# Performance work log

Hardware: AMD Instinct MI355X
Metric: run time of the kernel (lower is better)

Reference implementation:

```python
import jax, jax.numpy as jnp
import numpy as np
import math

LOG_EPS = -1000.0   # matches LOG_EPS in the torch source
NEG = -1e9          # stand-in for -inf (grad-safe)
T_MIN, T_MAX = 0.1, 1.0
GUMBEL_RATIO = 0.5  # gumbel_temperature_ratio forward arg (scalar float)


def setup_inputs() -> dict:
    key = jax.random.key(0)
    k1, k2, k3 = jax.random.split(key, 3)
    B, I, J, D = 4, 96, 384, 256
    return {
        "text_embeddings": jax.random.normal(k1, (B, I, D), jnp.float32),
        "mel_embeddings": jax.random.normal(k2, (B, J, D), jnp.float32),
        "gumbel_noise_u": jax.random.uniform(k3, (B, I, J), jnp.float32,
                                             minval=1e-6, maxval=1.0 - 1e-6),
        "text_mask": jnp.ones((B, I), dtype=bool),
        "mel_mask": jnp.ones((B, J), dtype=bool),
    }


def _soft_alignment(text_embeddings, mel_embeddings, gumbel_noise_u, text_mask, mel_mask):
    B, I, Dt = text_embeddings.shape
    _, J, Dm = mel_embeddings.shape

    # energy (B, I, J) = bmm / sqrt(D_text * D_mel)
    energy = jnp.einsum('bid,bjd->bij', text_embeddings, mel_embeddings) / math.sqrt(Dt * Dm)
    # gumbel noise + temperature
    temperature = T_MIN + (T_MAX - T_MIN) * GUMBEL_RATIO
    noise = -jnp.log(-jnp.log(gumbel_noise_u))
    energy = (energy + noise) / temperature

    len_t = text_mask.sum(1)  # (B,)
    len_m = mel_mask.sum(1)   # (B,)
    j_idx = jnp.arange(J)

    # invalid triangular mask (B, I, J, K): boundary j must not precede previous boundary k
    tri = j_idx[:, None] < j_idx[None, :]                       # (J, K)
    invalid = (tri[None, None]
               | ~text_mask[:, :, None, None]
               | ~mel_mask[:, None, :, None]
               | ~mel_mask[:, None, None, :])
    # force_assign_last: last text token's boundary forced to the last mel frame
    last_i = jnp.arange(I)[None, :] == (len_t - 1)[:, None]     # (B, I)
    not_last_j = j_idx[None, :] != (len_m - 1)[:, None]         # (B, J)
    invalid = invalid | (last_i[:, :, None, None] & not_last_j[:, None, :, None])

    # log conditional prob P(B_i = j | B_{i-1} = k), normalized over j (axis=2)
    e4 = jnp.where(invalid, LOG_EPS, energy[..., None])         # (B, I, J, K)
    log_cond_prob = e4 - jax.nn.logsumexp(e4, axis=2, keepdims=True)
    # reverse logcumsumexp over j: log P(B_i >= j | B_{i-1} = k)
    geq = jnp.flip(jax.lax.cumlogsumexp(jnp.flip(log_cond_prob, 2), axis=2), 2)
    geq = jnp.where(invalid, LOG_EPS, geq)

    # forward DP: B_ij (B, I+1, J+1), B_ij[:,0,0] = 0
    row0 = jnp.full((B, J + 1), NEG).at[:, 0].set(0.0)
    jj = jnp.arange(1, J + 1)

    def step(prev, inp):
        i, lcp = inp                                            # lcp: (B, J, K=J)
        # B_ij[b,i,j] = lse_k B_ij[b,i-1,k] + log_cond_prob[b,i-1,j-1,k]
        vals = jax.nn.logsumexp(prev[:, None, :-1] + lcp, axis=2)  # (B, J)
        window = (jj >= i) & (jj <= J - I + i + 1)              # only j in [i, J-I+i+1] written
        new = jnp.where(window[None, :], vals, NEG)
        new = jnp.concatenate([jnp.full((B, 1), NEG), new], axis=1)
        return new, new

    _, rows = jax.lax.scan(step, row0,
                           (jnp.arange(1, I + 1), jnp.swapaxes(log_cond_prob, 0, 1)))
    Bij = jnp.concatenate([row0[:, None, :], jnp.swapaxes(rows, 0, 1)], axis=1)  # (B, I+1, J+1)

    prob = Bij[:, :-1, :-1]                                     # (B, I, K)
    # log P(B_{i-1} < j <= B_i) = lse_k prob[b,i,k] + geq[b,i,j,k]
    log_boundary = jax.nn.logsumexp(prob[:, :, None, :] + geq, axis=3)  # (B, I, J)
    return log_boundary


def reference(text_embeddings, mel_embeddings, gumbel_noise_u, text_mask, mel_mask):
    soft = _soft_alignment(text_embeddings, mel_embeddings, gumbel_noise_u,
                           text_mask, mel_mask)
    # expanded text embeddings (B, J, D_text)
    expanded = jnp.einsum('bij,bid->bjd', jnp.exp(soft), text_embeddings)
    return soft, expanded
```

## Files before the change

### kernel.cpp

```cpp
#include <hip/hip_runtime.h>
#include <hip/hip_bf16.h>
#include <math.h>

#define B_ 4
#define I_ 96
#define J_ 384
#define D_ 256
#define NEG_     -1000000000.0f
#define NEGINF_  -3.0e38f
#define INV_TEMP_ (1.0f/0.55f)
#define LOG2E_   1.4426950408889634f
#define LN2_     0.6931471805599453f
#define LOGEPS2_ (-1000.0f*LOG2E_)

__device__ __forceinline__ float lse2(float a, float b) {
    float m = fmaxf(a, b);
    float d = fminf(a, b) - m;
    return m + __log2f(1.0f + __builtin_exp2f(d));
}

template<int CTRL, int RMASK = 0xF>
__device__ __forceinline__ float dpp_id(float x) {
    return __int_as_float(__builtin_amdgcn_update_dpp(
        __float_as_int(NEGINF_), __float_as_int(x), CTRL, RMASK, 0xF, false));
}
__device__ __forceinline__ float rdlane(float x, int l_const) {
    return __int_as_float(__builtin_amdgcn_readlane(__float_as_int(x), l_const));
}

__device__ __forceinline__ float wave_incl_prefix_lse(float x) {
    x = lse2(x, dpp_id<0x111>(x));
    x = lse2(x, dpp_id<0x112>(x));
    x = lse2(x, dpp_id<0x114>(x));
    x = lse2(x, dpp_id<0x118>(x));
    x = lse2(x, dpp_id<0x142, 0xa>(x));
    x = lse2(x, dpp_id<0x143, 0xc>(x));
    return x;
}
__device__ __forceinline__ float wave_incl_suffix_lse(float x, int lane) {
    x = lse2(x, dpp_id<0x101>(x));
    x = lse2(x, dpp_id<0x102>(x));
    x = lse2(x, dpp_id<0x104>(x));
    x = lse2(x, dpp_id<0x108>(x));
    float t1 = rdlane(x, 16), t2 = rdlane(x, 32), t3 = rdlane(x, 48);
    int row = lane >> 4;
    float u23 = lse2(t2, t3);
    float add = (row == 3) ? NEGINF_ : (row == 2) ? t3
              : (row == 1) ? u23 : lse2(t1, u23);
    return lse2(x, add);
}
__device__ __forceinline__ float combine_pre(const float* p, int w) {
    float l01 = lse2(p[0], p[1]);
    float l23 = lse2(p[2], p[3]);
    float P3 = lse2(l01, p[2]);
    float P4 = lse2(l01, l23);
    float P5 = lse2(P4, p[4]);
    return (w == 0) ? NEGINF_ : (w == 1) ? p[0] : (w == 2) ? l01
         : (w == 3) ? P3 : (w == 4) ? P4 : P5;
}
__device__ __forceinline__ float combine_suf(const float* s, int w) {
    float h45 = lse2(s[4], s[5]);
    float h23 = lse2(s[2], s[3]);
    float S3 = lse2(s[3], h45);
    float S2 = lse2(h23, h45);
    float S1 = lse2(s[1], S2);
    return (w == 5) ? NEGINF_ : (w == 4) ? s[5] : (w == 3) ? h45
         : (w == 2) ? S3 : (w == 1) ? S2 : S1;
}

__global__ __launch_bounds__(384) void k_energy(
    const float* __restrict__ text, const float* __restrict__ mel,
    const float* __restrict__ gum, float* __restrict__ Sarr,
    float* __restrict__ Earr)
{
    const int i = blockIdx.x, b = blockIdx.y;
    const int tid = threadIdx.x, lane = tid & 63, w = tid >> 6;
    __shared__ float4 tex4[D_/4];
    __shared__ float wtot[6];

    if (tid < D_/4)
        tex4[tid] = ((const float4*)(text + ((size_t)b*I_ + i)*D_))[tid];
    __syncthreads();

    const int j = tid;
    const float4* mrow = (const float4*)(mel + ((size_t)b*J_ + j)*D_);
    float acc = 0.f;
    #pragma unroll 8
    for (int d4 = 0; d4 < D_/4; ++d4) {
        float4 m4 = mrow[d4];
        float4 t4 = tex4[d4];
        acc += t4.x*m4.x + t4.y*m4.y + t4.z*m4.z + t4.w*m4.w;
    }
    float u = gum[((size_t)b*I_ + i)*J_ + j];
    float noise = -__logf(-__logf(u));
    float e2 = (acc * (1.0f/256.0f) + noise) * (INV_TEMP_ * LOG2E_);

    float sincl = wave_incl_suffix_lse(e2, lane);
    if (lane == 0) wtot[w] = sincl;
    __syncthreads();
    float sw = combine_suf(wtot, w);
    size_t off = ((size_t)b*I_ + i)*J_ + j;
    Sarr[off] = lse2(sincl, sw);
    Earr[off] = e2;
}

__global__ __launch_bounds__(64) void k_dp(
    const float* __restrict__ Sarr, const float* __restrict__ Earr,
    float* __restrict__ prob)
{
    const int b = blockIdx.x;
    const int lane = threadIdx.x;
    const int k0 = lane * 6;
    const float* Sb = Sarr + (size_t)b*I_*J_;
    const float* Eb = Earr + (size_t)b*I_*J_;
    float* Pb = prob + (size_t)b*I_*J_;

    float prev[6];
    #pragma unroll
    for (int t = 0; t < 6; ++t) {
        int k = k0 + t;
        float v0 = (k == 0) ? 0.0f : NEG_;
        prev[t] = v0;
        Pb[k] = v0;
    }

    float SA[6], EA[6], SBf[6], EBf[6];
    #pragma unroll
    for (int t = 0; t < 6; ++t) {
        int k = k0 + t;
        SA[t] = Sb[k];
        EA[t] = Eb[(k == 0) ? 0 : k - 1];
    }
    #pragma unroll
    for (int t = 0; t < 6; ++t) {
        int k = k0 + t;
        SBf[t] = Sb[(size_t)1*J_ + k];
        EBf[t] = Eb[(size_t)1*J_ + ((k == 0) ? 0 : k - 1)];
    }

    auto STEP = [&](int i, float* Sx, float* Ex, int loadrow) {
        float v[6], Ecur[6];
        #pragma unroll
        for (int t = 0; t < 6; ++t) { v[t] = prev[t] - Sx[t]; Ecur[t] = Ex[t]; }
        if (loadrow >= 0) {
            #pragma unroll
            for (int t = 0; t < 6; ++t) {
                int k = k0 + t;
                Sx[t] = Sb[(size_t)loadrow*J_ + k];
                Ex[t] = Eb[(size_t)loadrow*J_ + ((k == 0) ? 0 : k - 1)];
            }
        }
        float p[6];
        p[0] = v[0];
        #pragma unroll
        for (int t = 1; t < 6; ++t) p[t] = lse2(p[t-1], v[t]);
        float inc = wave_incl_prefix_lse(p[5]);
        float pexcl = dpp_id<0x138>(inc);
        float nv[6];
        nv[0] = pexcl + Ecur[0];
        #pragma unroll
        for (int t = 1; t < 6; ++t) nv[t] = lse2(pexcl, p[t-1]) + Ecur[t];
        float* Prow = Pb + (size_t)i*J_;
        #pragma unroll
        for (int t = 0; t < 6; ++t) {
            int k = k0 + t;
            bool win = (k >= i) && (k <= 289 + i);
            float val = win ? nv[t] : NEG_;
            prev[t] = val;
            Prow[k] = val;
        }
    };

    int i = 1;
    for (; i + 1 <= I_-1; i += 2) {
        STEP(i,     SA,  EA,  (i + 1 <= I_-2) ? i + 1 : -1);
        STEP(i + 1, SBf, EBf, (i + 2 <= I_-2) ? i + 2 : -1);
    }
    if (i == I_-1) STEP(i, SA, EA, -1);
}

__global__ __launch_bounds__(384) void k_soft(
    float* __restrict__ probsoft,
    const float* __restrict__ Sarr)
{
    const int i = blockIdx.x, b = blockIdx.y;
    const int tid = threadIdx.x, lane = tid & 63, w = tid >> 6;
    const int j = tid;
    __shared__ float tot[12];
    float* Row = probsoft + ((size_t)b*I_ + i)*J_;
    float p = Row[j];

    if (i == I_-1) {
        float sincl = wave_incl_suffix_lse(p, lane);
        if (lane == 0) tot[w] = sincl;
        __syncthreads();
        float m = tot[0];
        #pragma unroll
        for (int t = 1; t < 6; ++t) m = lse2(m, tot[t]);
        Row[j] = (j == J_-1) ? LN2_ * m : LN2_ * m - 1000.0f;
        return;
    }

    float S6 = Sarr[((size_t)b*I_ + i)*J_ + j];
    float v = p - S6;
    float qincl = wave_incl_prefix_lse(v);
    float tsuf  = wave_incl_suffix_lse(p, lane);
    if (lane == 63) tot[w] = qincl;
    if (lane == 0)  tot[6 + w] = tsuf;
    __syncthreads();
    float pt[6], st[6];
    #pragma unroll
    for (int t = 0; t < 6; ++t) { pt[t] = tot[t]; st[t] = tot[6+t]; }
    float Qful = lse2(combine_pre(pt, w), qincl);
    float Texw = dpp_id<0x130>(tsuf);
    float Texc = lse2(combine_suf(st, w), Texw);
    Row[j] = LN2_ * lse2(Qful + S6, Texc + LOGEPS2_);
}

__global__ __launch_bounds__(256) void k_expand(
    const float* __restrict__ soft, const float* __restrict__ text,
    float* __restrict__ out2)
{
    const int j = blockIdx.x, b = blockIdx.y;
    const int tid = threadIdx.x;
    __shared__ float wsh[I_];
    if (tid < I_) wsh[tid] = __expf(soft[((size_t)b*I_ + tid)*J_ + j]);
    __syncthreads();
    float acc = 0.f;
    const float* tcol = text + (size_t)b*I_*D_ + tid;
    #pragma unroll 8
    for (int i = 0; i < I_; ++i) acc += wsh[i] * tcol[(size_t)i*D_];
    out2[((size_t)b*J_ + j)*D_ + tid] = acc;
}

extern "C" void kernel_launch(void* const* d_in, const int* in_sizes, int n_in,
                              void* d_out, int out_size, void* d_ws, size_t ws_size,
                              hipStream_t stream) {
    const float* text = (const float*)d_in[0];
    const float* mel  = (const float*)d_in[1];
    const float* gum  = (const float*)d_in[2];

    float* out    = (float*)d_out;
    float* soft   = out;
    float* out2   = out + (size_t)B_*I_*J_;
    float* Sarr   = out2;
    float* Earr   = out2 + (size_t)B_*I_*J_;
    float* prob   = soft;

    k_energy<<<dim3(I_, B_), 384, 0, stream>>>(text, mel, gum, Sarr, Earr);
    k_dp    <<<dim3(B_),      64, 0, stream>>>(Sarr, Earr, prob);
    k_soft  <<<dim3(I_, B_), 384, 0, stream>>>(prob, Sarr);
    k_expand<<<dim3(J_, B_), 256, 0, stream>>>(soft, text, out2);
}
```

Baseline: 160.6 us.

## Tile energy and expand kernels, stage DP inputs in LDS as packed fp16

The energy kernel now computes six text rows per block, reusing each mel load across them, and rebuilds the per-row suffix log-sum-exp as an in-lane tree plus a wave scan. The DP kernel first preloads the whole per-batch S/E table into shared memory as packed fp16 pairs, so the serial 95-step recurrence reads from LDS instead of global memory. Its in-lane prefix scan is also reorganised into a shallower tree. The expand kernel handles eight output columns per block, reusing each text load across them. The fp16 storage of S and E lowers precision in the recurrence, and the roughly 147 KB LDS buffer limits the DP kernel to one block per CU.

```diff
diff --git a/kernel.cpp b/kernel.cpp
--- a/kernel.cpp
+++ b/kernel.cpp
@@ -1,5 +1,5 @@
 #include <hip/hip_runtime.h>
-#include <hip/hip_bf16.h>
+#include <hip/hip_fp16.h>
 #include <math.h>
 
 #define B_ 4
@@ -73,48 +73,88 @@
     const float* __restrict__ gum, float* __restrict__ Sarr,
     float* __restrict__ Earr)
 {
-    const int i = blockIdx.x, b = blockIdx.y;
+    const int ib = blockIdx.x * 6, b = blockIdx.y;
     const int tid = threadIdx.x, lane = tid & 63, w = tid >> 6;
-    __shared__ float4 tex4[D_/4];
-    __shared__ float wtot[6];
-
-    if (tid < D_/4)
-        tex4[tid] = ((const float4*)(text + ((size_t)b*I_ + i)*D_))[tid];
+    __shared__ float4 tex4[6][D_/4];
+    __shared__ float e2l[6][J_];
+
+    {
+        int r = tid >> 6, c = tid & 63;
+        tex4[r][c] = ((const float4*)(text + ((size_t)b*I_ + ib + r)*D_))[c];
+    }
     __syncthreads();
 
     const int j = tid;
     const float4* mrow = (const float4*)(mel + ((size_t)b*J_ + j)*D_);
-    float acc = 0.f;
-    #pragma unroll 8
+    float acc[6] = {0.f,0.f,0.f,0.f,0.f,0.f};
+    #pragma unroll 4
     for (int d4 = 0; d4 < D_/4; ++d4) {
         float4 m4 = mrow[d4];
-        float4 t4 = tex4[d4];
-        acc += t4.x*m4.x + t4.y*m4.y + t4.z*m4.z + t4.w*m4.w;
-    }
-    float u = gum[((size_t)b*I_ + i)*J_ + j];
-    float noise = -__logf(-__logf(u));
-    float e2 = (acc * (1.0f/256.0f) + noise) * (INV_TEMP_ * LOG2E_);
-
-    float sincl = wave_incl_suffix_lse(e2, lane);
-    if (lane == 0) wtot[w] = sincl;
-    __syncthreads();
-    float sw = combine_suf(wtot, w);
-    size_t off = ((size_t)b*I_ + i)*J_ + j;
-    Sarr[off] = lse2(sincl, sw);
-    Earr[off] = e2;
-}
-
-__global__ __launch_bounds__(64) void k_dp(
+        #pragma unroll
+        for (int r = 0; r < 6; ++r) {
+            float4 t4 = tex4[r][d4];
+            acc[r] += t4.x*m4.x + t4.y*m4.y + t4.z*m4.z + t4.w*m4.w;
+        }
+    }
+    #pragma unroll
+    for (int r = 0; r < 6; ++r) {
+        float u = gum[((size_t)b*I_ + ib + r)*J_ + j];
+        float noise = -__logf(-__logf(u));
+        e2l[r][j] = (acc[r] * (1.0f/256.0f) + noise) * (INV_TEMP_ * LOG2E_);
+    }
+    __syncthreads();
+
+    const int k0 = lane * 6;
+    float x[6];
+    #pragma unroll
+    for (int t = 0; t < 6; ++t) x[t] = e2l[w][k0 + t];
+    float s1[6], s2[6], sfx[6];
+    #pragma unroll
+    for (int t = 0; t < 5; ++t) s1[t] = lse2(x[t], x[t+1]);
+    s1[5] = x[5];
+    #pragma unroll
+    for (int t = 0; t < 4; ++t) s2[t] = lse2(s1[t], s1[t+2]);
+    s2[4] = s1[4]; s2[5] = s1[5];
+    sfx[0] = lse2(s2[0], s2[4]);
+    sfx[1] = lse2(s2[1], s2[5]);
+    #pragma unroll
+    for (int t = 2; t < 6; ++t) sfx[t] = s2[t];
+    float incl = wave_incl_suffix_lse(sfx[0], lane);
+    float excl = dpp_id<0x130>(incl);
+    size_t rowoff = ((size_t)b*I_ + ib + w)*J_ + k0;
+    #pragma unroll
+    for (int t = 0; t < 6; ++t) {
+        Sarr[rowoff + t] = lse2(sfx[t], excl);
+        Earr[rowoff + t] = x[t];
+    }
+}
+
+__global__ __launch_bounds__(384) void k_dp(
     const float* __restrict__ Sarr, const float* __restrict__ Earr,
     float* __restrict__ prob)
 {
+    __shared__ unsigned int SE[I_*J_];
     const int b = blockIdx.x;
-    const int lane = threadIdx.x;
-    const int k0 = lane * 6;
+    const int tid = threadIdx.x;
     const float* Sb = Sarr + (size_t)b*I_*J_;
     const float* Eb = Earr + (size_t)b*I_*J_;
     float* Pb = prob + (size_t)b*I_*J_;
 
+    {
+        const int k = tid, km1 = (k == 0) ? 0 : k - 1;
+        #pragma unroll 4
+        for (int r = 0; r < I_; ++r) {
+            float s = Sb[(size_t)r*J_ + k];
+            float e = Eb[(size_t)r*J_ + km1];
+            unsigned int u = ((unsigned int)__half_as_ushort(__float2half(e)) << 16)
+                           |  (unsigned int)__half_as_ushort(__float2half(s));
+            SE[r*J_ + k] = u;
+        }
+    }
+    __syncthreads();
+    if (tid >= 64) return;
+
+    const int lane = tid, k0 = lane * 6;
     float prev[6];
     #pragma unroll
     for (int t = 0; t < 6; ++t) {
@@ -123,43 +163,38 @@
         prev[t] = v0;
         Pb[k] = v0;
     }
-
-    float SA[6], EA[6], SBf[6], EBf[6];
-    #pragma unroll
-    for (int t = 0; t < 6; ++t) {
-        int k = k0 + t;
-        SA[t] = Sb[k];
-        EA[t] = Eb[(k == 0) ? 0 : k - 1];
-    }
-    #pragma unroll
-    for (int t = 0; t < 6; ++t) {
-        int k = k0 + t;
-        SBf[t] = Sb[(size_t)1*J_ + k];
-        EBf[t] = Eb[(size_t)1*J_ + ((k == 0) ? 0 : k - 1)];
-    }
-
-    auto STEP = [&](int i, float* Sx, float* Ex, int loadrow) {
-        float v[6], Ecur[6];
-        #pragma unroll
-        for (int t = 0; t < 6; ++t) { v[t] = prev[t] - Sx[t]; Ecur[t] = Ex[t]; }
-        if (loadrow >= 0) {
-            #pragma unroll
-            for (int t = 0; t < 6; ++t) {
-                int k = k0 + t;
-                Sx[t] = Sb[(size_t)loadrow*J_ + k];
-                Ex[t] = Eb[(size_t)loadrow*J_ + ((k == 0) ? 0 : k - 1)];
-            }
-        }
-        float p[6];
-        p[0] = v[0];
-        #pragma unroll
-        for (int t = 1; t < 6; ++t) p[t] = lse2(p[t-1], v[t]);
+    uint2 ca, cb, cc;
+    {
+        const uint2* p = (const uint2*)&SE[k0];
+        ca = p[0]; cb = p[1]; cc = p[2];
+    }
+    for (int i = 1; i <= I_-1; ++i) {
+        const uint2* pn = (const uint2*)&SE[(size_t)i*J_ + k0];
+        uint2 na = pn[0], nb = pn[1], nc = pn[2];
+        unsigned int uw[6] = { ca.x, ca.y, cb.x, cb.y, cc.x, cc.y };
+        float v[6], E6[6];
+        #pragma unroll
+        for (int t = 0; t < 6; ++t) {
+            float S = __half2float(__ushort_as_half((unsigned short)(uw[t] & 0xffff)));
+            E6[t]   = __half2float(__ushort_as_half((unsigned short)(uw[t] >> 16)));
+            v[t] = prev[t] - S;
+        }
+        float p1[6], p2[6], p[6];
+        p1[0] = v[0];
+        #pragma unroll
+        for (int t = 1; t < 6; ++t) p1[t] = lse2(v[t-1], v[t]);
+        p2[0] = p1[0]; p2[1] = p1[1];
+        #pragma unroll
+        for (int t = 2; t < 6; ++t) p2[t] = lse2(p1[t-2], p1[t]);
+        p[0] = p2[0]; p[1] = p2[1]; p[2] = p2[2]; p[3] = p2[3];
+        p[4] = lse2(p2[0], p2[4]);
+        p[5] = lse2(p2[1], p2[5]);
         float inc = wave_incl_prefix_lse(p[5]);
         float pexcl = dpp_id<0x138>(inc);
         float nv[6];
-        nv[0] = pexcl + Ecur[0];
-        #pragma unroll
-        for (int t = 1; t < 6; ++t) nv[t] = lse2(pexcl, p[t-1]) + Ecur[t];
+        nv[0] = pexcl + E6[0];
+        #pragma unroll
+        for (int t = 1; t < 6; ++t) nv[t] = lse2(pexcl, p[t-1]) + E6[t];
         float* Prow = Pb + (size_t)i*J_;
         #pragma unroll
         for (int t = 0; t < 6; ++t) {
@@ -169,14 +204,8 @@
             prev[t] = val;
             Prow[k] = val;
         }
-    };
-
-    int i = 1;
-    for (; i + 1 <= I_-1; i += 2) {
-        STEP(i,     SA,  EA,  (i + 1 <= I_-2) ? i + 1 : -1);
-        STEP(i + 1, SBf, EBf, (i + 2 <= I_-2) ? i + 2 : -1);
-    }
-    if (i == I_-1) STEP(i, SA, EA, -1);
+        ca = na; cb = nb; cc = nc;
+    }
 }
 
 __global__ __launch_bounds__(384) void k_soft(
@@ -221,16 +250,25 @@
     const float* __restrict__ soft, const float* __restrict__ text,
     float* __restrict__ out2)
 {
-    const int j = blockIdx.x, b = blockIdx.y;
+    const int jb = blockIdx.x * 8, b = blockIdx.y;
     const int tid = threadIdx.x;
-    __shared__ float wsh[I_];
-    if (tid < I_) wsh[tid] = __expf(soft[((size_t)b*I_ + tid)*J_ + j]);
-    __syncthreads();
-    float acc = 0.f;
+    __shared__ float wsh[8][I_];
+    for (int n = tid; n < 8*I_; n += 256) {
+        int jj = n / I_, ii = n % I_;
+        wsh[jj][ii] = __expf(soft[((size_t)b*I_ + ii)*J_ + jb + jj]);
+    }
+    __syncthreads();
+    float acc[8] = {0.f,0.f,0.f,0.f,0.f,0.f,0.f,0.f};
     const float* tcol = text + (size_t)b*I_*D_ + tid;
-    #pragma unroll 8
-    for (int i = 0; i < I_; ++i) acc += wsh[i] * tcol[(size_t)i*D_];
-    out2[((size_t)b*J_ + j)*D_ + tid] = acc;
+    #pragma unroll 4
+    for (int ii = 0; ii < I_; ++ii) {
+        float tv = tcol[(size_t)ii*D_];
+        #pragma unroll
+        for (int jj = 0; jj < 8; ++jj) acc[jj] += wsh[jj][ii] * tv;
+    }
+    #pragma unroll
+    for (int jj = 0; jj < 8; ++jj)
+        out2[((size_t)b*J_ + jb + jj)*D_ + tid] = acc[jj];
 }
 
 extern "C" void kernel_launch(void* const* d_in, const int* in_sizes, int n_in,
@@ -247,8 +285,8 @@
     float* Earr   = out2 + (size_t)B_*I_*J_;
     float* prob   = soft;
 
-    k_energy<<<dim3(I_, B_), 384, 0, stream>>>(text, mel, gum, Sarr, Earr);
-    k_dp    <<<dim3(B_),      64, 0, stream>>>(Sarr, Earr, prob);
-    k_soft  <<<dim3(I_, B_), 384, 0, stream>>>(prob, Sarr);
-    k_expand<<<dim3(J_, B_), 256, 0, stream>>>(soft, text, out2);
-}
+    k_energy<<<dim3(I_/6, B_), 384, 0, stream>>>(text, mel, gum, Sarr, Earr);
+    k_dp    <<<dim3(B_),       384, 0, stream>>>(Sarr, Earr, prob);
+    k_soft  <<<dim3(I_, B_),   384, 0, stream>>>(prob, Sarr);
+    k_expand<<<dim3(J_/8, B_), 256, 0, stream>>>(soft, text, out2);
+}
```

Result: slower. 169.9 us (+5.8%).
